# Kernel tuning notes

Measured on AMD Instinct MI355X. Metric: run time of the kernel, lower is better.

The kernel has to match this reference:

```python
import jax, jax.numpy as jnp
import numpy as np

N = 50000      # n_nodes
E = 300000     # n_edges
R = 32         # n_relations
D = 256        # embedding_dim
H = 128        # bilstm_hidden_size (2H == D so gate dims line up, as the source requires)
I = 64         # input_dim (time-series feature dim)
B = 4096       # batch
S = 50         # seq_len
HOPS = 2       # context_hops


def setup_inputs() -> dict:
    key = jax.random.key(0)
    ks = jax.random.split(key, 20)
    sc = 0.02
    inp = {
        "ts": jax.random.normal(ks[0], (B, S, I), jnp.float32),
        "node_emb": jax.random.normal(ks[1], (N, D), jnp.float32) * sc,
        "rel_w": jax.random.normal(ks[2], (R, D), jnp.float32) * sc + 1.0,
        "gate_W": jax.random.normal(ks[3], (D, 2 * D), jnp.float32) * sc,
        "gate_b": jnp.zeros((D,), jnp.float32),
        "risk_W1": jax.random.normal(ks[4], (D, D), jnp.float32) * sc,
        "risk_b1": jnp.zeros((D,), jnp.float32),
        "risk_W2": jax.random.normal(ks[5], (D, D), jnp.float32) * sc,
        "risk_b2": jnp.zeros((D,), jnp.float32),
        # BiLSTM encoder params (torch gate order i,f,g,o), fwd + bwd directions
        "Wih_f": jax.random.normal(ks[6], (4 * H, I), jnp.float32) * sc,
        "Whh_f": jax.random.normal(ks[7], (4 * H, H), jnp.float32) * sc,
        "b_f": jnp.zeros((4 * H,), jnp.float32),
        "Wih_b": jax.random.normal(ks[8], (4 * H, I), jnp.float32) * sc,
        "Whh_b": jax.random.normal(ks[9], (4 * H, H), jnp.float32) * sc,
        "b_b": jnp.zeros((4 * H,), jnp.float32),
        "edge_index": jax.random.randint(ks[10], (2, E), 0, N, jnp.int32),
        "edge_type": jax.random.randint(ks[11], (E,), 0, R, jnp.int32),
        "node_indexes": jax.random.randint(ks[12], (B,), 0, N, jnp.int32),
    }
    return inp


def _lstm_dir(x, Wih, Whh, b, reverse):
    # x: [B, S, I] -> outputs [B, S, H]
    def step(carry, xt):
        h, c = carry
        g = xt @ Wih.T + h @ Whh.T + b          # [B, 4H]
        i, f, gg, o = jnp.split(g, 4, axis=-1)
        c = jax.nn.sigmoid(f) * c + jax.nn.sigmoid(i) * jnp.tanh(gg)
        h = jax.nn.sigmoid(o) * jnp.tanh(c)
        return (h, c), h
    h0 = jnp.zeros((x.shape[0], Whh.shape[1]), x.dtype)
    xs = jnp.swapaxes(x, 0, 1)                   # [S, B, I]
    _, hs = jax.lax.scan(step, (h0, h0), xs, reverse=reverse)
    return jnp.swapaxes(hs, 0, 1)                # [B, S, H]


def _gcn(emb, head, tail, edge_type, rel_w, n_hops):
    # relation-weighted multi-hop message passing: gather -> relation scale -> scatter-mean
    deg = jax.ops.segment_sum(jnp.ones((head.shape[0],), emb.dtype), head, num_segments=N)
    deg = jnp.clip(deg, 1.0)[:, None]
    out = emb
    acc = emb
    for _ in range(n_hops):
        msg = out[tail] * rel_w[edge_type]                      # [E, D]
        out = jax.ops.segment_sum(msg, head, num_segments=N) / deg
        acc = acc + out
    return acc / (n_hops + 1.0)


def reference(ts, node_emb, rel_w, gate_W, gate_b, risk_W1, risk_b1, risk_W2,
              risk_b2, Wih_f, Whh_f, b_f, Wih_b, Whh_b, b_b,
              edge_index, edge_type, node_indexes):
    head, tail = edge_index[0], edge_index[1]
    all_emb = _gcn(node_emb, head, tail, edge_type, rel_w, HOPS)
    struct = all_emb[node_indexes]                              # [B, D]
    # BiLSTM encoder, temporal embedding = mean over time of [B,S,2H]
    hf = _lstm_dir(ts, Wih_f, Whh_f, b_f, reverse=False)
    hb = _lstm_dir(ts, Wih_b, Whh_b, b_b, reverse=True)
    temporal = jnp.concatenate([hf, hb], axis=-1).mean(axis=1)  # [B, 2H] == [B, D]
    cat = jnp.concatenate([struct, temporal], axis=-1)          # [B, 2D]
    gate = jax.nn.sigmoid(cat @ gate_W.T + gate_b)              # [B, D]
    merged = gate * struct + (1.0 - gate) * temporal
    risk = jnp.tanh(merged @ risk_W1.T + risk_b1) @ risk_W2.T + risk_b2
    return jax.nn.sigmoid(risk.sum(axis=-1))                    # [B]
```

## Files before the change

kernel.cpp:

```cpp
#include <hip/hip_runtime.h>

#define N_NODES 50000
#define N_EDGES 300000
#define DIM 256
#define HID 128
#define INP 64
#define BATCH 4096
#define SEQ 50
#define SCAN_BLOCKS 196

typedef float f32x2 __attribute__((ext_vector_type(2)));
typedef float f32x4 __attribute__((ext_vector_type(4)));
typedef __bf16 bf16x2 __attribute__((ext_vector_type(2)));
typedef __bf16 bf16x4 __attribute__((ext_vector_type(4)));
typedef __bf16 bf16x8 __attribute__((ext_vector_type(8)));

#define L2E  1.4426950408889634f
#define L2E2 2.8853900817779268f

__device__ __forceinline__ float sigmoidf_(float x) {
    return __builtin_amdgcn_rcpf(1.0f + __expf(-x));
}
__device__ __forceinline__ float tanhf_(float x) {
    return 1.0f - 2.0f * __builtin_amdgcn_rcpf(1.0f + __expf(2.0f * x));
}
__device__ __forceinline__ float sigp_(float y) {
    return __builtin_amdgcn_rcpf(1.0f + __builtin_amdgcn_exp2f(-y));
}
__device__ __forceinline__ float tanhp_(float y) {
    return 1.0f - 2.0f * __builtin_amdgcn_rcpf(1.0f + __builtin_amdgcn_exp2f(y));
}
__device__ __forceinline__ float tanhc_(float x) {
    return 1.0f - 2.0f * __builtin_amdgcn_rcpf(1.0f + __builtin_amdgcn_exp2f(x * L2E2));
}

__device__ __forceinline__ void barrier_lds_only() {
    asm volatile("s_waitcnt lgkmcnt(0)" ::: "memory");
    __builtin_amdgcn_s_barrier();
}

__global__ void k_prep(const float* __restrict__ Wih_f, const float* __restrict__ Whh_f,
                       const float* __restrict__ Wih_b, const float* __restrict__ Whh_b,
                       const float* __restrict__ gate_W, const float* __restrict__ risk_W1,
                       const float* __restrict__ risk_W2, const float* __restrict__ risk_b2,
                       const float* __restrict__ node_emb,
                       __bf16* __restrict__ w2frag, __bf16* __restrict__ gwp,
                       __bf16* __restrict__ w1p, float* __restrict__ w2s,
                       int* __restrict__ deg, int* __restrict__ flagi,
                       __bf16* __restrict__ embh) {
    __shared__ float red[256];
    int bid = blockIdx.x, tid = threadIdx.x;
    if (bid < 768) {
        int idx = bid * 256 + tid;
        int dir = idx / 98304;
        int rem = idx % 98304;
        int frag = rem >> 9;
        int within = rem & 511;
        int lane = within >> 3, j = within & 7;
        int kc = frag % 6;
        int wg = frag / 6;
        int g = wg & 3, w = wg >> 2;
        int n = g * 128 + w * 16 + (lane & 15);
        int k = kc * 32 + (lane >> 4) * 8 + j;
        const float* Wih = dir ? Wih_b : Wih_f;
        const float* Whh = dir ? Whh_b : Whh_f;
        float v = (k < 64) ? Wih[n * 64 + k] : Whh[n * 128 + (k - 64)];
        float sc = (g == 2) ? L2E2 : L2E;
        w2frag[idx] = (__bf16)(v * sc);
    } else if (bid < 1280) {
        int idx = (bid - 768) * 256 + tid;
        int frag = idx >> 9, within = idx & 511;
        int lane = within >> 3, j = within & 7;
        int kc = frag % 16, T = frag / 16;
        int n = T * 16 + (lane & 15);
        int k = kc * 32 + (lane >> 4) * 8 + j;
        gwp[idx] = (__bf16)gate_W[(size_t)n * 512 + k];
    } else if (bid < 1536) {
        int idx = (bid - 1280) * 256 + tid;
        int frag = idx >> 9, within = idx & 511;
        int lane = within >> 3, j = within & 7;
        int kc = frag % 8, T = frag / 8;
        int n = T * 16 + (lane & 15);
        int k = kc * 32 + (lane >> 4) * 8 + j;
        w1p[idx] = (__bf16)risk_W1[(size_t)n * 256 + k];
    } else if (bid == 1536) {
        int k = tid;
        float s = 0.0f;
        for (int n = 0; n < 256; n++) s += risk_W2[(size_t)n * 256 + k];
        w2s[k] = s;
        red[k] = risk_b2[k];
        __syncthreads();
        for (int st = 128; st > 0; st >>= 1) {
            if (k < st) red[k] += red[k + st];
            __syncthreads();
        }
        if (k == 0) w2s[256] = red[0];
    } else if (bid < 1733) {
        int i = (bid - 1537) * 256 + tid;
        if (i < N_NODES) deg[i] = 0;
    } else if (bid < 1782) {
        int i = (bid - 1733) * 256 + tid;
        flagi[i] = 0;
    } else {
        int idx = (bid - 1782) * 2048 + tid * 8;
        f32x4 a = *(const f32x4*)(node_emb + idx);
        f32x4 b = *(const f32x4*)(node_emb + idx + 4);
        bf16x8 o;
        o[0] = (__bf16)a.x; o[1] = (__bf16)a.y; o[2] = (__bf16)a.z; o[3] = (__bf16)a.w;
        o[4] = (__bf16)b.x; o[5] = (__bf16)b.y; o[6] = (__bf16)b.z; o[7] = (__bf16)b.w;
        *(bf16x8*)(embh + idx) = o;
    }
}


__global__ void k_hist(const int* __restrict__ head, int* __restrict__ deg) {
    int e = blockIdx.x * 256 + threadIdx.x;
    if (e < N_EDGES) atomicAdd(&deg[head[e]], 1);
}

__global__ void k_bsum(const int* __restrict__ deg, int* __restrict__ bsum) {
    __shared__ int red[256];
    int n = blockIdx.x * 256 + threadIdx.x;
    red[threadIdx.x] = (n < N_NODES) ? deg[n] : 0;
    __syncthreads();
    for (int st = 128; st > 0; st >>= 1) {
        if (threadIdx.x < st) red[threadIdx.x] += red[threadIdx.x + st];
        __syncthreads();
    }
    if (threadIdx.x == 0) bsum[blockIdx.x] = red[0];
}

__global__ void k_scan2(const int* __restrict__ deg, const int* __restrict__ bsum,
                        int* __restrict__ offsets, int* __restrict__ cursor) {
    __shared__ int s[256];
    __shared__ int sb[256];
    int i = threadIdx.x;
    int n = blockIdx.x * 256 + i;
    int v = (n < N_NODES) ? deg[n] : 0;
    s[i] = v;
    sb[i] = (i < SCAN_BLOCKS) ? bsum[i] : 0;
    __syncthreads();
    for (int st = 1; st < 256; st <<= 1) {
        int add = (i >= st) ? s[i - st] : 0;
        int addb = (i >= st) ? sb[i - st] : 0;
        __syncthreads();
        s[i] += add;
        sb[i] += addb;
        __syncthreads();
    }
    int boff = (blockIdx.x > 0) ? sb[blockIdx.x - 1] : 0;
    if (n < N_NODES) {
        int off = boff + s[i] - v;
        offsets[n] = off;
        cursor[n] = off;
    }
    if (n == 0) offsets[N_NODES] = N_EDGES;
}

__global__ void k_place(const int* __restrict__ head, const int* __restrict__ tail,
                        const int* __restrict__ etype, int* __restrict__ cursor,
                        int* __restrict__ sorted) {
    int e = blockIdx.x * 256 + threadIdx.x;
    if (e >= N_EDGES) return;
    int h = head[e];
    int pos = atomicAdd(&cursor[h], 1);
    sorted[pos] = tail[e] | (etype[e] << 16);
}

__global__ void k_flag(const int* __restrict__ nidx, const int* __restrict__ offsets,
                       const int* __restrict__ sorted, char* __restrict__ flag) {
    int tid = threadIdx.x;
    int w = tid >> 6, lane = tid & 63;
    int b = blockIdx.x * 4 + w;
    int n = nidx[b];
    if (lane == 0) flag[n] = 1;
    int s = offsets[n], e = offsets[n + 1];
    for (int j = s + lane; j < e; j += 64) flag[sorted[j] & 0xFFFF] = 1;
}

__global__ void k_gather(const int* __restrict__ offsets, const int* __restrict__ sorted,
                         const float* __restrict__ relw, const __bf16* __restrict__ srch,
                         const char* __restrict__ flag, __bf16* __restrict__ dst) {
    int tid = threadIdx.x;
    int w = tid >> 6, lane = tid & 63;
    int n = blockIdx.x * 4 + w;
    if (n >= N_NODES) return;
    if (!flag[n]) return;
    int s = offsets[n], e = offsets[n + 1];
    f32x4 acc0 = (f32x4){0.f, 0.f, 0.f, 0.f};
    f32x4 acc1 = (f32x4){0.f, 0.f, 0.f, 0.f};
    f32x4 acc2 = (f32x4){0.f, 0.f, 0.f, 0.f};
    f32x4 acc3 = (f32x4){0.f, 0.f, 0.f, 0.f};
    int j = s;
    for (; j + 4 <= e; j += 4) {
        int p0 = sorted[j], p1 = sorted[j + 1], p2 = sorted[j + 2], p3 = sorted[j + 3];
        bf16x4 v0 = *(const bf16x4*)(srch + (size_t)(p0 & 0xFFFF) * DIM + lane * 4);
        bf16x4 v1 = *(const bf16x4*)(srch + (size_t)(p1 & 0xFFFF) * DIM + lane * 4);
        bf16x4 v2 = *(const bf16x4*)(srch + (size_t)(p2 & 0xFFFF) * DIM + lane * 4);
        bf16x4 v3 = *(const bf16x4*)(srch + (size_t)(p3 & 0xFFFF) * DIM + lane * 4);
        f32x4 f0 = (f32x4){(float)v0[0], (float)v0[1], (float)v0[2], (float)v0[3]};
        f32x4 f1 = (f32x4){(float)v1[0], (float)v1[1], (float)v1[2], (float)v1[3]};
        f32x4 f2 = (f32x4){(float)v2[0], (float)v2[1], (float)v2[2], (float)v2[3]};
        f32x4 f3 = (f32x4){(float)v3[0], (float)v3[1], (float)v3[2], (float)v3[3]};
        acc0 += f0 * *(const f32x4*)(relw + (p0 >> 16) * DIM + lane * 4);
        acc1 += f1 * *(const f32x4*)(relw + (p1 >> 16) * DIM + lane * 4);
        acc2 += f2 * *(const f32x4*)(relw + (p2 >> 16) * DIM + lane * 4);
        acc3 += f3 * *(const f32x4*)(relw + (p3 >> 16) * DIM + lane * 4);
    }
    for (; j < e; j++) {
        int p0 = sorted[j];
        bf16x4 v0 = *(const bf16x4*)(srch + (size_t)(p0 & 0xFFFF) * DIM + lane * 4);
        f32x4 f0 = (f32x4){(float)v0[0], (float)v0[1], (float)v0[2], (float)v0[3]};
        acc0 += f0 * *(const f32x4*)(relw + (p0 >> 16) * DIM + lane * 4);
    }
    acc0 = (acc0 + acc1) + (acc2 + acc3);
    float inv = 1.0f / fmaxf((float)(e - s), 1.0f);
    acc0 *= inv;
    bf16x4 o;
    o[0] = (__bf16)acc0.x; o[1] = (__bf16)acc0.y; o[2] = (__bf16)acc0.z; o[3] = (__bf16)acc0.w;
    *(bf16x4*)(dst + (size_t)n * DIM + lane * 4) = o;
}

__launch_bounds__(512)
__global__ void k_lstm(const float* __restrict__ ts, const __bf16* __restrict__ w2frag,
                       const float* __restrict__ b_f, const float* __restrict__ b_b,
                       float* __restrict__ temporal) {
    int dir = blockIdx.y;
    int btile = blockIdx.x;
    int tid = threadIdx.x;
    int w = tid >> 6;
    int lane = tid & 63;
    int col = lane & 15, quad = lane >> 4;

    __shared__ __align__(16) __bf16 SA[2 * 16 * 200];
    __shared__ __align__(16) __bf16 SB[2 * 16 * 200];

    for (int i = tid; i < 2048; i += 512) {
        int m = i >> 7, k = i & 127;
        SA[m * 200 + 64 + k] = (__bf16)0.0f;
        SB[m * 200 + 64 + k] = (__bf16)0.0f;
    }

    const float* bias = dir ? b_b : b_f;
    f32x4 bva[4];
#pragma unroll
    for (int g = 0; g < 4; g++) {
        float b = bias[g * 128 + w * 16 + col] * ((g == 2) ? L2E2 : L2E);
        bva[g] = (f32x4){b, b, b, b};
    }

    const __bf16* wbase = w2frag + (size_t)dir * 98304 + (size_t)w * 12288;
    bf16x8 wreg[24];
#pragma unroll
    for (int f = 0; f < 24; f++) {
        wreg[f] = *(const bf16x8*)(wbase + (f << 9) + lane * 8);
    }

    int sm = tid >> 5, sc = (tid & 31) * 2;
    const float* xbA = ts + ((size_t)(btile * 32 + sm) * SEQ) * INP + sc;
    const float* xbB = ts + ((size_t)(btile * 32 + 16 + sm) * SEQ) * INP + sc;
    int t0i = dir ? (SEQ - 1) : 0;
    int t1i = dir ? (SEQ - 2) : 1;
    {
        f32x2 xa = *(const f32x2*)(xbA + (size_t)t0i * INP);
        f32x2 xb = *(const f32x2*)(xbB + (size_t)t0i * INP);
        bf16x2 va; va[0] = (__bf16)xa.x; va[1] = (__bf16)xa.y;
        bf16x2 vb; vb[0] = (__bf16)xb.x; vb[1] = (__bf16)xb.y;
        *(bf16x2*)&SA[sm * 200 + sc] = va;
        *(bf16x2*)&SB[sm * 200 + sc] = vb;
    }
    f32x2 xpreA = *(const f32x2*)(xbA + (size_t)t1i * INP);
    f32x2 xpreB = *(const f32x2*)(xbB + (size_t)t1i * INP);
    int xdelta = dir ? -INP : INP;
    const float* pA = xbA + (size_t)(dir ? (SEQ - 3) : 2) * INP;
    const float* pB = xbB + (size_t)(dir ? (SEQ - 3) : 2) * INP;

    f32x4 cA = (f32x4){0.f, 0.f, 0.f, 0.f}, hsA = cA;
    f32x4 cB = cA, hsB = cA;
    f32x4 accA[4], accB[4];
    int hwr = quad * 4 * 200 + 64 + w * 16 + col;
    int ard = col * 200 + quad * 8;
    barrier_lds_only();

    {
        bf16x8 a0 = *(const bf16x8*)&SA[ard];
#pragma unroll
        for (int g = 0; g < 4; g++)
            accA[g] = __builtin_amdgcn_mfma_f32_16x16x32_bf16(a0, wreg[g * 6], bva[g], 0, 0, 0);
    }
#pragma unroll
    for (int kc = 1; kc < 6; kc++) {
        bf16x8 a0 = *(const bf16x8*)&SA[ard + kc * 32];
#pragma unroll
        for (int g = 0; g < 4; g++)
            accA[g] = __builtin_amdgcn_mfma_f32_16x16x32_bf16(a0, wreg[g * 6 + kc], accA[g], 0, 0, 0);
    }

    for (int t = 0; t < SEQ; t++) {
        int cb = (t & 1) * 3200;
        int nb = ((t + 1) & 1) * 3200;

        f32x2 xnA;
        bool ld = (t + 2 < SEQ);
        if (ld) { xnA = *(const f32x2*)pA; pA += xdelta; }
        {
            bf16x8 a0 = *(const bf16x8*)&SB[cb + ard];
#pragma unroll
            for (int g = 0; g < 4; g++)
                accB[g] = __builtin_amdgcn_mfma_f32_16x16x32_bf16(a0, wreg[g * 6], bva[g], 0, 0, 0);
        }
#pragma unroll
        for (int kc = 1; kc < 6; kc++) {
            bf16x8 a0 = *(const bf16x8*)&SB[cb + ard + kc * 32];
#pragma unroll
            for (int g = 0; g < 4; g++)
                accB[g] = __builtin_amdgcn_mfma_f32_16x16x32_bf16(a0, wreg[g * 6 + kc], accB[g], 0, 0, 0);
        }
#pragma unroll
        for (int r = 0; r < 4; r++) {
            float c = sigp_(accA[1][r]) * cA[r] + sigp_(accA[0][r]) * tanhp_(accA[2][r]);
            float h = sigp_(accA[3][r]) * tanhc_(c);
            cA[r] = c;
            hsA[r] += h;
            SA[nb + hwr + r * 200] = (__bf16)h;
        }
        if (t + 1 < SEQ) {
            bf16x2 v; v[0] = (__bf16)xpreA.x; v[1] = (__bf16)xpreA.y;
            *(bf16x2*)&SA[nb + sm * 200 + sc] = v;
            if (ld) xpreA = xnA;
        }
        barrier_lds_only();

        f32x2 xnB;
        if (ld) { xnB = *(const f32x2*)pB; pB += xdelta; }
        if (t + 1 < SEQ) {
            {
                bf16x8 a0 = *(const bf16x8*)&SA[nb + ard];
#pragma unroll
                for (int g = 0; g < 4; g++)
                    accA[g] = __builtin_amdgcn_mfma_f32_16x16x32_bf16(a0, wreg[g * 6], bva[g], 0, 0, 0);
            }
#pragma unroll
            for (int kc = 1; kc < 6; kc++) {
                bf16x8 a0 = *(const bf16x8*)&SA[nb + ard + kc * 32];
#pragma unroll
                for (int g = 0; g < 4; g++)
                    accA[g] = __builtin_amdgcn_mfma_f32_16x16x32_bf16(a0, wreg[g * 6 + kc], accA[g], 0, 0, 0);
            }
        }
#pragma unroll
        for (int r = 0; r < 4; r++) {
            float c = sigp_(accB[1][r]) * cB[r] + sigp_(accB[0][r]) * tanhp_(accB[2][r]);
            float h = sigp_(accB[3][r]) * tanhc_(c);
            cB[r] = c;
            hsB[r] += h;
            SB[nb + hwr + r * 200] = (__bf16)h;
        }
        if (t + 1 < SEQ) {
            bf16x2 v; v[0] = (__bf16)xpreB.x; v[1] = (__bf16)xpreB.y;
            *(bf16x2*)&SB[nb + sm * 200 + sc] = v;
            if (ld) xpreB = xnB;
        }
        barrier_lds_only();
    }

#pragma unroll
    for (int r = 0; r < 4; r++) {
        int j = w * 16 + col;
        int bA = btile * 32 + quad * 4 + r;
        int bB = bA + 16;
        temporal[(size_t)bA * 256 + dir * 128 + j] = hsA[r] * (1.0f / SEQ);
        temporal[(size_t)bB * 256 + dir * 128 + j] = hsB[r] * (1.0f / SEQ);
    }
}

__global__ void k_gather2(const int* __restrict__ nidx, const int* __restrict__ offsets,
                          const int* __restrict__ sorted, const float* __restrict__ relw,
                          const __bf16* __restrict__ out1h, const __bf16* __restrict__ embh,
                          float* __restrict__ structb) {
    int tid = threadIdx.x;
    int w = tid >> 6, lane = tid & 63;
    int b = blockIdx.x * 4 + w;
    int n = nidx[b];
    int s = offsets[n], e = offsets[n + 1];
    f32x4 acc0 = (f32x4){0.f, 0.f, 0.f, 0.f};
    f32x4 acc1 = (f32x4){0.f, 0.f, 0.f, 0.f};
    f32x4 acc2 = (f32x4){0.f, 0.f, 0.f, 0.f};
    f32x4 acc3 = (f32x4){0.f, 0.f, 0.f, 0.f};
    int j = s;
    for (; j + 4 <= e; j += 4) {
        int p0 = sorted[j], p1 = sorted[j + 1], p2 = sorted[j + 2], p3 = sorted[j + 3];
        bf16x4 v0 = *(const bf16x4*)(out1h + (size_t)(p0 & 0xFFFF) * DIM + lane * 4);
        bf16x4 v1 = *(const bf16x4*)(out1h + (size_t)(p1 & 0xFFFF) * DIM + lane * 4);
        bf16x4 v2 = *(const bf16x4*)(out1h + (size_t)(p2 & 0xFFFF) * DIM + lane * 4);
        bf16x4 v3 = *(const bf16x4*)(out1h + (size_t)(p3 & 0xFFFF) * DIM + lane * 4);
        f32x4 f0 = (f32x4){(float)v0[0], (float)v0[1], (float)v0[2], (float)v0[3]};
        f32x4 f1 = (f32x4){(float)v1[0], (float)v1[1], (float)v1[2], (float)v1[3]};
        f32x4 f2 = (f32x4){(float)v2[0], (float)v2[1], (float)v2[2], (float)v2[3]};
        f32x4 f3 = (f32x4){(float)v3[0], (float)v3[1], (float)v3[2], (float)v3[3]};
        acc0 += f0 * *(const f32x4*)(relw + (p0 >> 16) * DIM + lane * 4);
        acc1 += f1 * *(const f32x4*)(relw + (p1 >> 16) * DIM + lane * 4);
        acc2 += f2 * *(const f32x4*)(relw + (p2 >> 16) * DIM + lane * 4);
        acc3 += f3 * *(const f32x4*)(relw + (p3 >> 16) * DIM + lane * 4);
    }
    for (; j < e; j++) {
        int p0 = sorted[j];
        bf16x4 v0 = *(const bf16x4*)(out1h + (size_t)(p0 & 0xFFFF) * DIM + lane * 4);
        f32x4 f0 = (f32x4){(float)v0[0], (float)v0[1], (float)v0[2], (float)v0[3]};
        acc0 += f0 * *(const f32x4*)(relw + (p0 >> 16) * DIM + lane * 4);
    }
    acc0 = (acc0 + acc1) + (acc2 + acc3);
    float inv = 1.0f / fmaxf((float)(e - s), 1.0f);
    f32x4 o2 = acc0 * inv;
    bf16x4 eh = *(const bf16x4*)(embh + (size_t)n * DIM + lane * 4);
    bf16x4 o1h = *(const bf16x4*)(out1h + (size_t)n * DIM + lane * 4);
    f32x4 e0 = (f32x4){(float)eh[0], (float)eh[1], (float)eh[2], (float)eh[3]};
    f32x4 o1 = (f32x4){(float)o1h[0], (float)o1h[1], (float)o1h[2], (float)o1h[3]};
    *(f32x4*)(structb + (size_t)b * DIM + lane * 4) = (e0 + o1 + o2) * (1.0f / 3.0f);
}


__launch_bounds__(256)
__global__ void k_head(const float* __restrict__ structb, const float* __restrict__ temporal,
                       const __bf16* __restrict__ gwp, const __bf16* __restrict__ w1p,
                       const float* __restrict__ gate_b, const float* __restrict__ risk_b1,
                       const float* __restrict__ w2s, float* __restrict__ out) {
    int bt = blockIdx.x;
    int tid = threadIdx.x;
    int w = tid >> 6, lane = tid & 63;
    int col = lane & 15, quad = lane >> 4;

    __shared__ __align__(16) __bf16 cat[16][520];
    __shared__ __align__(16) __bf16 mbuf[16][264];
    __shared__ float sacc[16];

    for (int i = tid; i < 16 * 512; i += 256) {
        int m = i >> 9, k = i & 511;
        int b = bt * 16 + m;
        float v = (k < 256) ? structb[(size_t)b * 256 + k]
                            : temporal[(size_t)b * 256 + (k - 256)];
        cat[m][k] = (__bf16)v;
    }
    if (tid < 16) sacc[tid] = 0.0f;
    __syncthreads();

    f32x4 acc[4];
#pragma unroll
    for (int ct = 0; ct < 4; ct++) {
        float b = gate_b[w * 64 + ct * 16 + col];
        acc[ct] = (f32x4){b, b, b, b};
    }
#pragma unroll
    for (int kc = 0; kc < 16; kc++) {
        bf16x8 a = *(const bf16x8*)&cat[col][kc * 32 + quad * 8];
#pragma unroll
        for (int ct = 0; ct < 4; ct++) {
            bf16x8 bf = *(const bf16x8*)(gwp + (((w * 4 + ct) * 16 + kc) << 9) + lane * 8);
            acc[ct] = __builtin_amdgcn_mfma_f32_16x16x32_bf16(a, bf, acc[ct], 0, 0, 0);
        }
    }
#pragma unroll
    for (int ct = 0; ct < 4; ct++) {
        int n = w * 64 + ct * 16 + col;
#pragma unroll
        for (int r = 0; r < 4; r++) {
            int m = quad * 4 + r;
            int b = bt * 16 + m;
            float g = sigmoidf_(acc[ct][r]);
            float s = structb[(size_t)b * 256 + n];
            float tm = temporal[(size_t)b * 256 + n];
            mbuf[m][n] = (__bf16)(g * s + (1.0f - g) * tm);
        }
    }
    __syncthreads();

    f32x4 acc2[4];
#pragma unroll
    for (int ct = 0; ct < 4; ct++) {
        float b = risk_b1[w * 64 + ct * 16 + col];
        acc2[ct] = (f32x4){b, b, b, b};
    }
#pragma unroll
    for (int kc = 0; kc < 8; kc++) {
        bf16x8 a = *(const bf16x8*)&mbuf[col][kc * 32 + quad * 8];
#pragma unroll
        for (int ct = 0; ct < 4; ct++) {
            bf16x8 bf = *(const bf16x8*)(w1p + (((w * 4 + ct) * 8 + kc) << 9) + lane * 8);
            acc2[ct] = __builtin_amdgcn_mfma_f32_16x16x32_bf16(a, bf, acc2[ct], 0, 0, 0);
        }
    }
    float part[4] = {0.f, 0.f, 0.f, 0.f};
#pragma unroll
    for (int ct = 0; ct < 4; ct++) {
        int n = w * 64 + ct * 16 + col;
        float wv = w2s[n];
#pragma unroll
        for (int r = 0; r < 4; r++) {
            part[r] += tanhf_(acc2[ct][r]) * wv;
        }
    }
#pragma unroll
    for (int off = 1; off < 16; off <<= 1) {
#pragma unroll
        for (int r = 0; r < 4; r++) part[r] += __shfl_xor(part[r], off, 64);
    }
    if (col == 0) {
#pragma unroll
        for (int r = 0; r < 4; r++) atomicAdd(&sacc[quad * 4 + r], part[r]);
    }
    __syncthreads();
    if (tid < 16) out[bt * 16 + tid] = sigmoidf_(sacc[tid] + w2s[256]);
}


extern "C" void kernel_launch(void* const* d_in, const int* in_sizes, int n_in,
                              void* d_out, int out_size, void* d_ws, size_t ws_size,
                              hipStream_t stream) {
    const float* ts       = (const float*)d_in[0];
    const float* node_emb = (const float*)d_in[1];
    const float* rel_w    = (const float*)d_in[2];
    const float* gate_W   = (const float*)d_in[3];
    const float* gate_b   = (const float*)d_in[4];
    const float* risk_W1  = (const float*)d_in[5];
    const float* risk_b1  = (const float*)d_in[6];
    const float* risk_W2  = (const float*)d_in[7];
    const float* risk_b2  = (const float*)d_in[8];
    const float* Wih_f    = (const float*)d_in[9];
    const float* Whh_f    = (const float*)d_in[10];
    const float* b_f      = (const float*)d_in[11];
    const float* Wih_b    = (const float*)d_in[12];
    const float* Whh_b    = (const float*)d_in[13];
    const float* b_b      = (const float*)d_in[14];
    const int* edge_index = (const int*)d_in[15];
    const int* edge_type  = (const int*)d_in[16];
    const int* node_idx   = (const int*)d_in[17];
    const int* head = edge_index;
    const int* tail = edge_index + N_EDGES;
    float* out = (float*)d_out;

    char* ws = (char*)d_ws;
    const size_t o_deg      = 0;
    const size_t o_flagbuf  = 200704;
    const size_t o_bsum     = o_flagbuf + 50176;
    const size_t o_boff     = o_bsum + 1024;
    const size_t o_offsets  = o_boff + 1024;
    const size_t o_cursor   = o_offsets + 200960;
    const size_t o_sorted   = o_cursor + 200704;
    const size_t o_out1     = o_sorted + 1200128;
    const size_t o_embh     = o_out1 + 25600000;
    const size_t o_temporal = o_embh + 25600000;
    const size_t o_struct   = o_temporal + 4194304;
    const size_t o_gwp      = o_struct + 4194304;
    const size_t o_w1p      = o_gwp + 262144;
    const size_t o_w2s      = o_w1p + 131072;
    const size_t o_w2frag   = o_w2s + 2048;

    int*    deg      = (int*)(ws + o_deg);
    char*   flag     = (char*)(ws + o_flagbuf);
    int*    flagi    = (int*)(ws + o_flagbuf);
    int*    bsum     = (int*)(ws + o_bsum);
    int*    offsets  = (int*)(ws + o_offsets);
    int*    cursor   = (int*)(ws + o_cursor);
    int*    sorted   = (int*)(ws + o_sorted);
    __bf16* out1h    = (__bf16*)(ws + o_out1);
    __bf16* embh     = (__bf16*)(ws + o_embh);
    float*  temporal = (float*)(ws + o_temporal);
    float*  structb  = (float*)(ws + o_struct);
    __bf16* gwp      = (__bf16*)(ws + o_gwp);
    __bf16* w1p      = (__bf16*)(ws + o_w1p);
    float*  w2s      = (float*)(ws + o_w2s);
    __bf16* w2frag   = (__bf16*)(ws + o_w2frag);

    k_prep<<<8032, 256, 0, stream>>>(Wih_f, Whh_f, Wih_b, Whh_b, gate_W, risk_W1,
                                     risk_W2, risk_b2, node_emb, w2frag, gwp, w1p,
                                     w2s, deg, flagi, embh);
    k_hist<<<(N_EDGES + 255) / 256, 256, 0, stream>>>(head, deg);
    k_bsum<<<SCAN_BLOCKS, 256, 0, stream>>>(deg, bsum);
    k_scan2<<<SCAN_BLOCKS, 256, 0, stream>>>(deg, bsum, offsets, cursor);
    k_place<<<(N_EDGES + 255) / 256, 256, 0, stream>>>(head, tail, edge_type, cursor, sorted);
    k_flag<<<BATCH / 4, 256, 0, stream>>>(node_idx, offsets, sorted, flag);
    k_gather<<<(N_NODES + 3) / 4, 256, 0, stream>>>(offsets, sorted, rel_w, embh, flag, out1h);
    k_lstm<<<dim3(BATCH / 32, 2), 512, 0, stream>>>(ts, w2frag, b_f, b_b, temporal);
    k_gather2<<<BATCH / 4, 256, 0, stream>>>(node_idx, offsets, sorted, rel_w, out1h, embh, structb);
    k_head<<<BATCH / 16, 256, 0, stream>>>(structb, temporal, gwp, w1p, gate_b, risk_b1, w2s, out);
}
```

Before: 312.7 us.

## Fuse CSR build and flag marking into one cooperative grid-sync kernel

Replaces the histogram, block-sum, scan, place and flag kernels (plus the zeroing done in prep) with a single cooperative kernel that uses grid.sync between phases. Neighbour flags are now set during edge placement by checking whether the head node is a batch node, instead of in a separate pass over the sorted adjacency. This removes several kernel launches and their gaps. In exchange it adds grid-wide barriers and needs all 1172 blocks co-resident, and the launch return code is not checked.

```diff
diff --git a/kernel.cpp b/kernel.cpp
--- a/kernel.cpp
+++ b/kernel.cpp
@@ -1,4 +1,7 @@
 #include <hip/hip_runtime.h>
+#include <hip/hip_cooperative_groups.h>
+
+namespace cg = cooperative_groups;
 
 #define N_NODES 50000
 #define N_EDGES 300000
@@ -8,6 +11,7 @@
 #define BATCH 4096
 #define SEQ 50
 #define SCAN_BLOCKS 196
+#define SORT_GRID 1172
 
 typedef float f32x2 __attribute__((ext_vector_type(2)));
 typedef float f32x4 __attribute__((ext_vector_type(4)));
@@ -46,7 +50,6 @@
                        const float* __restrict__ node_emb,
                        __bf16* __restrict__ w2frag, __bf16* __restrict__ gwp,
                        __bf16* __restrict__ w1p, float* __restrict__ w2s,
-                       int* __restrict__ deg, int* __restrict__ flagi,
                        __bf16* __restrict__ embh) {
     __shared__ float red[256];
     int bid = blockIdx.x, tid = threadIdx.x;
@@ -95,14 +98,8 @@
             __syncthreads();
         }
         if (k == 0) w2s[256] = red[0];
-    } else if (bid < 1733) {
-        int i = (bid - 1537) * 256 + tid;
-        if (i < N_NODES) deg[i] = 0;
-    } else if (bid < 1782) {
-        int i = (bid - 1733) * 256 + tid;
-        flagi[i] = 0;
     } else {
-        int idx = (bid - 1782) * 2048 + tid * 8;
+        int idx = (bid - 1537) * 2048 + tid * 8;
         f32x4 a = *(const f32x4*)(node_emb + idx);
         f32x4 b = *(const f32x4*)(node_emb + idx + 4);
         bf16x8 o;
@@ -112,70 +109,72 @@
     }
 }
 
-
-__global__ void k_hist(const int* __restrict__ head, int* __restrict__ deg) {
-    int e = blockIdx.x * 256 + threadIdx.x;
-    if (e < N_EDGES) atomicAdd(&deg[head[e]], 1);
-}
-
-__global__ void k_bsum(const int* __restrict__ deg, int* __restrict__ bsum) {
-    __shared__ int red[256];
-    int n = blockIdx.x * 256 + threadIdx.x;
-    red[threadIdx.x] = (n < N_NODES) ? deg[n] : 0;
-    __syncthreads();
-    for (int st = 128; st > 0; st >>= 1) {
-        if (threadIdx.x < st) red[threadIdx.x] += red[threadIdx.x + st];
-        __syncthreads();
-    }
-    if (threadIdx.x == 0) bsum[blockIdx.x] = red[0];
-}
-
-__global__ void k_scan2(const int* __restrict__ deg, const int* __restrict__ bsum,
-                        int* __restrict__ offsets, int* __restrict__ cursor) {
+__global__ void k_sort(const int* __restrict__ head, const int* __restrict__ tail,
+                       const int* __restrict__ etype, const int* __restrict__ nidx,
+                       int* __restrict__ deg, int* __restrict__ bsum,
+                       int* __restrict__ offsets, int* __restrict__ cursor,
+                       int* __restrict__ sorted, char* __restrict__ flagB,
+                       char* __restrict__ flagC) {
+    cg::grid_group grid = cg::this_grid();
+    int tid = threadIdx.x, bid = blockIdx.x;
+    int gidx = bid * 256 + tid;
+    const int GSTRIDE = SORT_GRID * 256;
+
+    int* flagBi = (int*)flagB;
+    int* flagCi = (int*)flagC;
+    for (int i = gidx; i < N_NODES; i += GSTRIDE) deg[i] = 0;
+    for (int i = gidx; i < 12544; i += GSTRIDE) { flagBi[i] = 0; flagCi[i] = 0; }
+    grid.sync();
+
+    if (gidx < N_EDGES) atomicAdd(&deg[head[gidx]], 1);
+    if (gidx < BATCH) { int n = nidx[gidx]; flagB[n] = 1; flagC[n] = 1; }
+    grid.sync();
+
     __shared__ int s[256];
     __shared__ int sb[256];
-    int i = threadIdx.x;
-    int n = blockIdx.x * 256 + i;
-    int v = (n < N_NODES) ? deg[n] : 0;
-    s[i] = v;
-    sb[i] = (i < SCAN_BLOCKS) ? bsum[i] : 0;
-    __syncthreads();
-    for (int st = 1; st < 256; st <<= 1) {
-        int add = (i >= st) ? s[i - st] : 0;
-        int addb = (i >= st) ? sb[i - st] : 0;
+    if (bid < SCAN_BLOCKS) {
+        int n = bid * 256 + tid;
+        int v = (n < N_NODES) ? deg[n] : 0;
+        s[tid] = v;
         __syncthreads();
-        s[i] += add;
-        sb[i] += addb;
+        for (int st = 128; st > 0; st >>= 1) {
+            if (tid < st) s[tid] += s[tid + st];
+            __syncthreads();
+        }
+        if (tid == 0) bsum[bid] = s[0];
+    }
+    grid.sync();
+
+    if (bid < SCAN_BLOCKS) {
+        int n = bid * 256 + tid;
+        int v = (n < N_NODES) ? deg[n] : 0;
+        s[tid] = v;
+        sb[tid] = (tid < SCAN_BLOCKS) ? bsum[tid] : 0;
         __syncthreads();
-    }
-    int boff = (blockIdx.x > 0) ? sb[blockIdx.x - 1] : 0;
-    if (n < N_NODES) {
-        int off = boff + s[i] - v;
-        offsets[n] = off;
-        cursor[n] = off;
-    }
-    if (n == 0) offsets[N_NODES] = N_EDGES;
-}
-
-__global__ void k_place(const int* __restrict__ head, const int* __restrict__ tail,
-                        const int* __restrict__ etype, int* __restrict__ cursor,
-                        int* __restrict__ sorted) {
-    int e = blockIdx.x * 256 + threadIdx.x;
-    if (e >= N_EDGES) return;
-    int h = head[e];
-    int pos = atomicAdd(&cursor[h], 1);
-    sorted[pos] = tail[e] | (etype[e] << 16);
-}
-
-__global__ void k_flag(const int* __restrict__ nidx, const int* __restrict__ offsets,
-                       const int* __restrict__ sorted, char* __restrict__ flag) {
-    int tid = threadIdx.x;
-    int w = tid >> 6, lane = tid & 63;
-    int b = blockIdx.x * 4 + w;
-    int n = nidx[b];
-    if (lane == 0) flag[n] = 1;
-    int s = offsets[n], e = offsets[n + 1];
-    for (int j = s + lane; j < e; j += 64) flag[sorted[j] & 0xFFFF] = 1;
+        for (int st = 1; st < 256; st <<= 1) {
+            int a = (tid >= st) ? s[tid - st] : 0;
+            int ab = (tid >= st) ? sb[tid - st] : 0;
+            __syncthreads();
+            s[tid] += a;
+            sb[tid] += ab;
+            __syncthreads();
+        }
+        int boff = (bid > 0) ? sb[bid - 1] : 0;
+        if (n < N_NODES) {
+            int off = boff + s[tid] - v;
+            offsets[n] = off;
+            cursor[n] = off;
+        }
+        if (n == 0) offsets[N_NODES] = N_EDGES;
+    }
+    grid.sync();
+
+    if (gidx < N_EDGES) {
+        int h = head[gidx];
+        int pos = atomicAdd(&cursor[h], 1);
+        sorted[pos] = tail[gidx] | (etype[gidx] << 16);
+        if (flagB[h]) flagC[tail[gidx]] = 1;
+    }
 }
 
 __global__ void k_gather(const int* __restrict__ offsets, const int* __restrict__ sorted,
@@ -554,10 +553,11 @@
     const size_t o_w1p      = o_gwp + 262144;
     const size_t o_w2s      = o_w1p + 131072;
     const size_t o_w2frag   = o_w2s + 2048;
+    const size_t o_flagB    = o_w2frag + 393216;
 
     int*    deg      = (int*)(ws + o_deg);
-    char*   flag     = (char*)(ws + o_flagbuf);
-    int*    flagi    = (int*)(ws + o_flagbuf);
+    char*   flagC    = (char*)(ws + o_flagbuf);
+    char*   flagB    = (char*)(ws + o_flagB);
     int*    bsum     = (int*)(ws + o_bsum);
     int*    offsets  = (int*)(ws + o_offsets);
     int*    cursor   = (int*)(ws + o_cursor);
@@ -571,15 +571,17 @@
     float*  w2s      = (float*)(ws + o_w2s);
     __bf16* w2frag   = (__bf16*)(ws + o_w2frag);
 
-    k_prep<<<8032, 256, 0, stream>>>(Wih_f, Whh_f, Wih_b, Whh_b, gate_W, risk_W1,
+    k_prep<<<7787, 256, 0, stream>>>(Wih_f, Whh_f, Wih_b, Whh_b, gate_W, risk_W1,
                                      risk_W2, risk_b2, node_emb, w2frag, gwp, w1p,
-                                     w2s, deg, flagi, embh);
-    k_hist<<<(N_EDGES + 255) / 256, 256, 0, stream>>>(head, deg);
-    k_bsum<<<SCAN_BLOCKS, 256, 0, stream>>>(deg, bsum);
-    k_scan2<<<SCAN_BLOCKS, 256, 0, stream>>>(deg, bsum, offsets, cursor);
-    k_place<<<(N_EDGES + 255) / 256, 256, 0, stream>>>(head, tail, edge_type, cursor, sorted);
-    k_flag<<<BATCH / 4, 256, 0, stream>>>(node_idx, offsets, sorted, flag);
-    k_gather<<<(N_NODES + 3) / 4, 256, 0, stream>>>(offsets, sorted, rel_w, embh, flag, out1h);
+                                     w2s, embh);
+    {
+        void* sargs[] = {(void*)&head, (void*)&tail, (void*)&edge_type, (void*)&node_idx,
+                         (void*)&deg, (void*)&bsum, (void*)&offsets, (void*)&cursor,
+                         (void*)&sorted, (void*)&flagB, (void*)&flagC};
+        hipLaunchCooperativeKernel((void*)k_sort, dim3(SORT_GRID), dim3(256),
+                                   sargs, 0, stream);
+    }
+    k_gather<<<(N_NODES + 3) / 4, 256, 0, stream>>>(offsets, sorted, rel_w, embh, flagC, out1h);
     k_lstm<<<dim3(BATCH / 32, 2), 512, 0, stream>>>(ts, w2frag, b_f, b_b, temporal);
     k_gather2<<<BATCH / 4, 256, 0, stream>>>(node_idx, offsets, sorted, rel_w, out1h, embh, structb);
     k_head<<<BATCH / 16, 256, 0, stream>>>(structb, temporal, gwp, w1p, gate_b, risk_b1, w2s, out);
```

After: 758.0 us. 142% more time.

## Fuse block-sum and flag marking into histogram and placement kernels

Applied to the files above, without the earlier changes.

Removes the separate k_bsum and k_flag launches. Block sums are now built with extra atomics in k_hist, batch nodes are flagged there too, and k_place marks the neighbours of flagged heads while it scatters edges. This saves two kernel launches and a reread of the sorted adjacency, at the cost of one more contended atomic per edge on the bsum array and a flag read in k_place. The extra flag and bsum buffers are zeroed in k_prep.

```diff
diff --git a/kernel.cpp b/kernel.cpp
--- a/kernel.cpp
+++ b/kernel.cpp
@@ -39,6 +39,7 @@
     __builtin_amdgcn_s_barrier();
 }
 
+
 __global__ void k_prep(const float* __restrict__ Wih_f, const float* __restrict__ Whh_f,
                        const float* __restrict__ Wih_b, const float* __restrict__ Whh_b,
                        const float* __restrict__ gate_W, const float* __restrict__ risk_W1,
@@ -46,7 +47,8 @@
                        const float* __restrict__ node_emb,
                        __bf16* __restrict__ w2frag, __bf16* __restrict__ gwp,
                        __bf16* __restrict__ w1p, float* __restrict__ w2s,
-                       int* __restrict__ deg, int* __restrict__ flagi,
+                       int* __restrict__ deg, int* __restrict__ flagCi,
+                       int* __restrict__ flagBi, int* __restrict__ bsum,
                        __bf16* __restrict__ embh) {
     __shared__ float red[256];
     int bid = blockIdx.x, tid = threadIdx.x;
@@ -100,9 +102,14 @@
         if (i < N_NODES) deg[i] = 0;
     } else if (bid < 1782) {
         int i = (bid - 1733) * 256 + tid;
-        flagi[i] = 0;
+        flagCi[i] = 0;
+    } else if (bid < 1831) {
+        int i = (bid - 1782) * 256 + tid;
+        flagBi[i] = 0;
+    } else if (bid == 1831) {
+        bsum[tid] = 0;
     } else {
-        int idx = (bid - 1782) * 2048 + tid * 8;
+        int idx = (bid - 1832) * 2048 + tid * 8;
         f32x4 a = *(const f32x4*)(node_emb + idx);
         f32x4 b = *(const f32x4*)(node_emb + idx + 4);
         bf16x8 o;
@@ -112,22 +119,20 @@
     }
 }
 
-
-__global__ void k_hist(const int* __restrict__ head, int* __restrict__ deg) {
+__global__ void k_hist(const int* __restrict__ head, const int* __restrict__ nidx,
+                       int* __restrict__ deg, int* __restrict__ bsum,
+                       char* __restrict__ flagB, char* __restrict__ flagC) {
     int e = blockIdx.x * 256 + threadIdx.x;
-    if (e < N_EDGES) atomicAdd(&deg[head[e]], 1);
-}
-
-__global__ void k_bsum(const int* __restrict__ deg, int* __restrict__ bsum) {
-    __shared__ int red[256];
-    int n = blockIdx.x * 256 + threadIdx.x;
-    red[threadIdx.x] = (n < N_NODES) ? deg[n] : 0;
-    __syncthreads();
-    for (int st = 128; st > 0; st >>= 1) {
-        if (threadIdx.x < st) red[threadIdx.x] += red[threadIdx.x + st];
-        __syncthreads();
-    }
-    if (threadIdx.x == 0) bsum[blockIdx.x] = red[0];
+    if (e < N_EDGES) {
+        int h = head[e];
+        atomicAdd(&deg[h], 1);
+        atomicAdd(&bsum[h >> 8], 1);
+    }
+    if (e < BATCH) {
+        int n = nidx[e];
+        flagB[n] = 1;
+        flagC[n] = 1;
+    }
 }
 
 __global__ void k_scan2(const int* __restrict__ deg, const int* __restrict__ bsum,
@@ -159,23 +164,15 @@
 
 __global__ void k_place(const int* __restrict__ head, const int* __restrict__ tail,
                         const int* __restrict__ etype, int* __restrict__ cursor,
-                        int* __restrict__ sorted) {
+                        int* __restrict__ sorted, const char* __restrict__ flagB,
+                        char* __restrict__ flagC) {
     int e = blockIdx.x * 256 + threadIdx.x;
     if (e >= N_EDGES) return;
     int h = head[e];
     int pos = atomicAdd(&cursor[h], 1);
-    sorted[pos] = tail[e] | (etype[e] << 16);
-}
-
-__global__ void k_flag(const int* __restrict__ nidx, const int* __restrict__ offsets,
-                       const int* __restrict__ sorted, char* __restrict__ flag) {
-    int tid = threadIdx.x;
-    int w = tid >> 6, lane = tid & 63;
-    int b = blockIdx.x * 4 + w;
-    int n = nidx[b];
-    if (lane == 0) flag[n] = 1;
-    int s = offsets[n], e = offsets[n + 1];
-    for (int j = s + lane; j < e; j += 64) flag[sorted[j] & 0xFFFF] = 1;
+    int t = tail[e];
+    sorted[pos] = t | (etype[e] << 16);
+    if (flagB[h]) flagC[t] = 1;
 }
 
 __global__ void k_gather(const int* __restrict__ offsets, const int* __restrict__ sorted,
@@ -554,10 +551,11 @@
     const size_t o_w1p      = o_gwp + 262144;
     const size_t o_w2s      = o_w1p + 131072;
     const size_t o_w2frag   = o_w2s + 2048;
+    const size_t o_flagB    = o_w2frag + 393216;
 
     int*    deg      = (int*)(ws + o_deg);
-    char*   flag     = (char*)(ws + o_flagbuf);
-    int*    flagi    = (int*)(ws + o_flagbuf);
+    char*   flagC    = (char*)(ws + o_flagbuf);
+    char*   flagB    = (char*)(ws + o_flagB);
     int*    bsum     = (int*)(ws + o_bsum);
     int*    offsets  = (int*)(ws + o_offsets);
     int*    cursor   = (int*)(ws + o_cursor);
@@ -571,15 +569,14 @@
     float*  w2s      = (float*)(ws + o_w2s);
     __bf16* w2frag   = (__bf16*)(ws + o_w2frag);
 
-    k_prep<<<8032, 256, 0, stream>>>(Wih_f, Whh_f, Wih_b, Whh_b, gate_W, risk_W1,
+    k_prep<<<8082, 256, 0, stream>>>(Wih_f, Whh_f, Wih_b, Whh_b, gate_W, risk_W1,
                                      risk_W2, risk_b2, node_emb, w2frag, gwp, w1p,
-                                     w2s, deg, flagi, embh);
-    k_hist<<<(N_EDGES + 255) / 256, 256, 0, stream>>>(head, deg);
-    k_bsum<<<SCAN_BLOCKS, 256, 0, stream>>>(deg, bsum);
+                                     w2s, deg, (int*)flagC, (int*)flagB, bsum, embh);
+    k_hist<<<(N_EDGES + 255) / 256, 256, 0, stream>>>(head, node_idx, deg, bsum, flagB, flagC);
     k_scan2<<<SCAN_BLOCKS, 256, 0, stream>>>(deg, bsum, offsets, cursor);
-    k_place<<<(N_EDGES + 255) / 256, 256, 0, stream>>>(head, tail, edge_type, cursor, sorted);
-    k_flag<<<BATCH / 4, 256, 0, stream>>>(node_idx, offsets, sorted, flag);
-    k_gather<<<(N_NODES + 3) / 4, 256, 0, stream>>>(offsets, sorted, rel_w, embh, flag, out1h);
+    k_place<<<(N_EDGES + 255) / 256, 256, 0, stream>>>(head, tail, edge_type, cursor,
+                                                       sorted, flagB, flagC);
+    k_gather<<<(N_NODES + 3) / 4, 256, 0, stream>>>(offsets, sorted, rel_w, embh, flagC, out1h);
     k_lstm<<<dim3(BATCH / 32, 2), 512, 0, stream>>>(ts, w2frag, b_f, b_b, temporal);
     k_gather2<<<BATCH / 4, 256, 0, stream>>>(node_idx, offsets, sorted, rel_w, out1h, embh, structb);
     k_head<<<BATCH / 16, 256, 0, stream>>>(structb, temporal, gwp, w1p, gate_b, risk_b1, w2s, out);
```

After: 476.2 us. 1.52x slower.
